# Kernel optimization log

Hardware: AMD Instinct MI355X
Metric: run time of the kernel (lower is better)

## Reference

```python
import jax, jax.numpy as jnp
import numpy as np

N_NODES = 100000
N_EDGES = 1600000
N_REL = 8
IN_CH = 64
HIDDEN = 64
OUT_CH = 32


def setup_inputs() -> dict:
    key = jax.random.key(0)
    ks = jax.random.split(key, 10)
    s_in = 1.0 / np.sqrt(IN_CH)
    s_h = 1.0 / np.sqrt(HIDDEN)
    return {
        "x": jax.random.normal(ks[0], (N_NODES, IN_CH), dtype=jnp.float32),
        "edge_index": jax.random.randint(ks[1], (2, N_EDGES), 0, N_NODES, dtype=jnp.int64),
        "edge_type": jax.random.randint(ks[2], (N_EDGES,), 0, N_REL, dtype=jnp.int64),
        "W0": jax.random.normal(ks[3], (N_REL, IN_CH, HIDDEN), dtype=jnp.float32) * s_in,
        "Q0": jax.random.normal(ks[4], (HIDDEN, 1), dtype=jnp.float32) * s_h,
        "K0": jax.random.normal(ks[5], (HIDDEN, 1), dtype=jnp.float32) * s_h,
        "b0": jnp.zeros((HIDDEN,), dtype=jnp.float32),
        "W1": jax.random.normal(ks[6], (N_REL, HIDDEN, OUT_CH), dtype=jnp.float32) * s_h,
        "Q1": jax.random.normal(ks[7], (OUT_CH, 1), dtype=jnp.float32) * (1.0 / np.sqrt(OUT_CH)),
        "K1": jax.random.normal(ks[8], (OUT_CH, 1), dtype=jnp.float32) * (1.0 / np.sqrt(OUT_CH)),
        "b1": jnp.zeros((OUT_CH,), dtype=jnp.float32),
    }


def rgat_conv(x, src, dst, et, W, Q, K, b, n_nodes):
    # relation-typed transform of all nodes: [R, N, out]
    xw = jnp.einsum("ni,rio->rno", x, W)
    # per-node, per-relation attention logits (heads=1, dim=1)
    q = jnp.einsum("rno,od->rnd", xw, Q)[..., 0]  # [R, N]
    k = jnp.einsum("rno,od->rnd", xw, K)[..., 0]  # [R, N]
    # additive self-attention, leaky_relu slope 0.2 (PyG RGATConv default)
    alpha = jax.nn.leaky_relu(q[et, dst] + k[et, src], negative_slope=0.2)  # [E]
    # across-relation segment softmax over incoming edges of each dst node
    amax = jax.ops.segment_max(alpha, dst, num_segments=n_nodes)
    a = jnp.exp(alpha - amax[dst])
    denom = jax.ops.segment_sum(a, dst, num_segments=n_nodes)
    a = a / (denom[dst] + 1e-16)
    # weighted scatter-add aggregation of transformed source features
    msg = a[:, None] * xw[et, src]  # [E, out]
    return jax.ops.segment_sum(msg, dst, num_segments=n_nodes) + b


def reference(x, edge_index, edge_type, W0, Q0, K0, b0, W1, Q1, K1, b1):
    src, dst = edge_index[0], edge_index[1]
    n = x.shape[0]
    h = rgat_conv(x, src, dst, edge_type, W0, Q0, K0, b0, n)
    h = jax.nn.relu(h)  # dropout p=0.0 -> identity
    out = rgat_conv(h, src, dst, edge_type, W1, Q1, K1, b1, n)
    return out
```

## Files before the change

kernel.cpp:

```cpp
#include <hip/hip_runtime.h>
#include <hip/hip_bf16.h>
#include <math.h>


#define CSR_CHUNK 8192

__global__ void k_bhist(const int* __restrict__ dst, int* __restrict__ bcount,
                        int E, int NB) {
    __shared__ int h[512];
    int t = threadIdx.x;
    for (int i = t; i < NB; i += 256) h[i] = 0;
    __syncthreads();
    int e0 = blockIdx.x * CSR_CHUNK;
    int e1 = min(e0 + CSR_CHUNK, E);
    for (int i = e0 + t; i < e1; i += 256) atomicAdd(&h[dst[i] >> 8], 1);
    __syncthreads();
    for (int i = t; i < NB; i += 256) {
        int c = h[i];
        if (c) atomicAdd(&bcount[i], c);
    }
}

__global__ void k_bscan(const int* __restrict__ bcount, int* __restrict__ bstart,
                        int* __restrict__ gcur, int* __restrict__ rowptr,
                        int NB, int N, int E) {
    __shared__ int s[512];
    int t = threadIdx.x;
    int v = (t < NB) ? bcount[t] : 0;
    s[t] = v;
    __syncthreads();
    for (int off = 1; off < 512; off <<= 1) {
        int a = (t >= off) ? s[t - off] : 0;
        __syncthreads();
        s[t] += a;
        __syncthreads();
    }
    int excl = s[t] - v;
    if (t < NB) {
        bstart[t] = excl;
        gcur[t] = excl;
    }
    if (t == 0) {
        bstart[NB] = E;
        rowptr[N] = E;
    }
}

__global__ void k_bscatter(const int* __restrict__ src, const int* __restrict__ dst,
                           const int* __restrict__ et, int* __restrict__ gcur,
                           unsigned* __restrict__ ebuf, int E, int NB) {
    __shared__ int h[512];
    __shared__ int basearr[512];
    int t = threadIdx.x;
    for (int i = t; i < NB; i += 256) h[i] = 0;
    __syncthreads();
    int e0 = blockIdx.x * CSR_CHUNK;
    int e1 = min(e0 + CSR_CHUNK, E);
    for (int i = e0 + t; i < e1; i += 256) atomicAdd(&h[dst[i] >> 8], 1);
    __syncthreads();
    for (int i = t; i < NB; i += 256) {
        int c = h[i];
        basearr[i] = c ? atomicAdd(&gcur[i], c) : 0;
        h[i] = 0;
    }
    __syncthreads();
    for (int i = e0 + t; i < e1; i += 256) {
        int d = dst[i];
        int b = d >> 8;
        int off = atomicAdd(&h[b], 1);
        ebuf[basearr[b] + off] =
            ((unsigned)(d & 255) << 20) | ((unsigned)et[i] << 17) | (unsigned)src[i];
    }
}

__global__ void k_bsort(const unsigned* __restrict__ ebuf, const int* __restrict__ bstart,
                        int* __restrict__ rowptr, int* __restrict__ csr, int N) {
    __shared__ int lh[256];
    __shared__ int ls[256];
    __shared__ int ss[256];
    int b = blockIdx.x, t = threadIdx.x;
    int e0 = bstart[b], e1 = bstart[b + 1];
    lh[t] = 0;
    __syncthreads();
    for (int i = e0 + t; i < e1; i += 256) atomicAdd(&lh[(ebuf[i] >> 20) & 255], 1);
    __syncthreads();
    int v = lh[t];
    ss[t] = v;
    __syncthreads();
    for (int off = 1; off < 256; off <<= 1) {
        int a = (t >= off) ? ss[t - off] : 0;
        __syncthreads();
        ss[t] += a;
        __syncthreads();
    }
    ls[t] = ss[t] - v;
    int node = b * 256 + t;
    if (node < N) rowptr[node] = e0 + ls[t];
    lh[t] = 0;
    __syncthreads();
    for (int i = e0 + t; i < e1; i += 256) {
        unsigned u = ebuf[i];
        int d = (u >> 20) & 255;
        int off = atomicAdd(&lh[d], 1);
        csr[e0 + ls[d] + off] = (int)(u & 0xFFFFF);
    }
}


__global__ void k_cast(const float4* __restrict__ in, ushort4* __restrict__ out, int n4) {
    int i = blockIdx.x * blockDim.x + threadIdx.x;
    if (i < n4) {
        float4 v = in[i];
        __hip_bfloat16 a = __float2bfloat16(v.x);
        __hip_bfloat16 b = __float2bfloat16(v.y);
        __hip_bfloat16 c = __float2bfloat16(v.z);
        __hip_bfloat16 d = __float2bfloat16(v.w);
        ushort4 o;
        o.x = *(unsigned short*)&a;
        o.y = *(unsigned short*)&b;
        o.z = *(unsigned short*)&c;
        o.w = *(unsigned short*)&d;
        out[i] = o;
    }
}


__global__ void k_wt2(const float* __restrict__ W, __hip_bfloat16* __restrict__ hi,
                      __hip_bfloat16* __restrict__ lo, int OUT, int total) {
    int t = blockIdx.x * blockDim.x + threadIdx.x;
    if (t < total) {
        int per = 64 * OUT;
        int r = t / per;
        int rem = t % per;
        int i = rem / OUT;
        int o = rem % OUT;
        float v = W[t];
        __hip_bfloat16 h = __float2bfloat16(v);
        __hip_bfloat16 l = __float2bfloat16(v - __bfloat162float(h));
        size_t idx = (size_t)o * 512 + i * 8 + r;
        hi[idx] = h;
        lo[idx] = l;
    }
}

__global__ void k_wqk(const float* W, const float* Qv, const float* Kv,
                      float* wq, float* wk, int OUT) {
    int t = blockIdx.x * blockDim.x + threadIdx.x;
    if (t < 8 * 64) {
        int r = t >> 6, i = t & 63;
        const float* wrow = W + ((size_t)r * 64 + i) * OUT;
        float a = 0.f, b = 0.f;
        for (int o = 0; o < OUT; o++) {
            float w = wrow[o];
            a += w * Qv[o];
            b += w * Kv[o];
        }
        wq[t] = a;
        wk[t] = b;
    }
}

__global__ void k_qk(const float* __restrict__ xin, const float* __restrict__ wq,
                     const float* __restrict__ wk, float* __restrict__ qn,
                     float* __restrict__ kn, int N) {
    __shared__ float sq[8 * 65], sk[8 * 65];
    int t = threadIdx.x;
    for (int idx = t; idx < 8 * 64; idx += blockDim.x) {
        int r = idx >> 6, i = idx & 63;
        sq[r * 65 + i] = wq[idx];
        sk[r * 65 + i] = wk[idx];
    }
    __syncthreads();
    int g = blockIdx.x * blockDim.x + t;
    if (g < N * 8) {
        int n = g >> 3, r = g & 7;
        const float* xp = xin + (size_t)n * 64;
        float qa = 0.f, ka = 0.f;
#pragma unroll
        for (int i = 0; i < 64; i++) {
            float xv = xp[i];
            qa += xv * sq[r * 65 + i];
            ka += xv * sk[r * 65 + i];
        }
        qn[g] = qa;
        kn[g] = ka;
    }
}

__global__ void k_agg2(const int* __restrict__ rowptr, const int* __restrict__ csr,
                       const float* __restrict__ qn, const float* __restrict__ kn,
                       const unsigned short* __restrict__ xb,
                       __hip_bfloat16* __restrict__ z, int N) {
    int wid = (blockIdx.x * blockDim.x + threadIdx.x) >> 6;
    int lane = threadIdx.x & 63;
    if (wid >= N) return;
    int r0 = rowptr[wid], r1 = rowptr[wid + 1];

    float qv = (lane < 8) ? qn[wid * 8 + lane] : 0.f;

    float denom = 0.f;
    float a0 = 0.f, a1 = 0.f, a2 = 0.f, a3 = 0.f;
    float a4 = 0.f, a5 = 0.f, a6 = 0.f, a7 = 0.f;

    for (int base = r0; base < r1; base += 64) {
        int s = base + lane;
        int pk = (s < r1) ? csr[s] : 0;
        int src = pk & 0x1FFFF;
        int rel = pk >> 17;
        float q = __shfl(qv, rel, 64);
        float tv = 0.f;
        if (s < r1) {
            float v = q + kn[src * 8 + rel];
            v = (v >= 0.f) ? v : 0.2f * v;
            tv = __expf(v);
        }
        float ts = tv;
#pragma unroll
        for (int off = 32; off > 0; off >>= 1) ts += __shfl_xor(ts, off, 64);
        denom += ts;

        int cnt = min(64, r1 - base);
        int tvi = (int)__float_as_uint(tv);
        for (int j = 0; j < cnt; j += 8) {
            unsigned p[8];
            float t[8];
#pragma unroll
            for (int u = 0; u < 8; u++) {
                p[u] = (unsigned)__builtin_amdgcn_readlane(pk, j + u);
                t[u] = __uint_as_float((unsigned)__builtin_amdgcn_readlane(tvi, j + u));
            }
            unsigned xu[8];
#pragma unroll
            for (int u = 0; u < 8; u++)
                xu[u] = (unsigned)xb[(size_t)(p[u] & 0x1FFFF) * 64 + lane];
#pragma unroll
            for (int u = 0; u < 8; u++) {
                float xv = __uint_as_float(xu[u] << 16);
                float tj = t[u];
                switch (p[u] >> 17) {
                    case 0: a0 += tj * xv; break;
                    case 1: a1 += tj * xv; break;
                    case 2: a2 += tj * xv; break;
                    case 3: a3 += tj * xv; break;
                    case 4: a4 += tj * xv; break;
                    case 5: a5 += tj * xv; break;
                    case 6: a6 += tj * xv; break;
                    case 7: a7 += tj * xv; break;
                }
            }
        }
    }

    float inv = 1.f / (denom + 1e-16f);
    unsigned short u[8];
    float av[8] = {a0, a1, a2, a3, a4, a5, a6, a7};
#pragma unroll
    for (int r = 0; r < 8; r++) {
        __hip_bfloat16 b = __float2bfloat16(av[r] * inv);
        u[r] = *(unsigned short*)&b;
    }
    uint4 pack;
    pack.x = (unsigned)u[0] | ((unsigned)u[1] << 16);
    pack.y = (unsigned)u[2] | ((unsigned)u[3] << 16);
    pack.z = (unsigned)u[4] | ((unsigned)u[5] << 16);
    pack.w = (unsigned)u[6] | ((unsigned)u[7] << 16);
    *(uint4*)((unsigned short*)z + (size_t)wid * 512 + lane * 8) = pack;
}

template <int OUT, bool RELU>
__global__ __launch_bounds__(256) void k_zw(
        const __hip_bfloat16* __restrict__ z,
        const __hip_bfloat16* __restrict__ wthi, const __hip_bfloat16* __restrict__ wtlo,
        const float* __restrict__ bias, float* __restrict__ xout,
        unsigned short* __restrict__ bout, int N) {
    using v8s = __attribute__((ext_vector_type(8))) short;
    using v4f = __attribute__((ext_vector_type(4))) float;
    constexpr int NT = OUT / 16;
    int wave = threadIdx.x >> 6;
    int lane = threadIdx.x & 63;
    int quad = lane >> 4;
    int l15 = lane & 15;
    int m0 = (blockIdx.x * 4 + wave) * 32;
    if (m0 >= N) return;

    v4f acc[NT][2];
#pragma unroll
    for (int nt = 0; nt < NT; nt++) {
        acc[nt][0] = (v4f){0.f, 0.f, 0.f, 0.f};
        acc[nt][1] = (v4f){0.f, 0.f, 0.f, 0.f};
    }

    const short* zp = (const short*)z;
    const short* wh = (const short*)wthi;
    const short* wl = (const short*)wtlo;
    int n0 = m0 + l15, n1 = m0 + 16 + l15;

    for (int k0 = 0; k0 < 512; k0 += 32) {
        int koff = k0 + quad * 8;
        v8s A0 = {}, A1 = {};
        if (n0 < N) A0 = *(const v8s*)(zp + (size_t)n0 * 512 + koff);
        if (n1 < N) A1 = *(const v8s*)(zp + (size_t)n1 * 512 + koff);
#pragma unroll
        for (int nt = 0; nt < NT; nt++) {
            v8s bh = *(const v8s*)(wh + (size_t)(nt * 16 + l15) * 512 + koff);
            v8s bl = *(const v8s*)(wl + (size_t)(nt * 16 + l15) * 512 + koff);
            acc[nt][0] = __builtin_amdgcn_mfma_f32_16x16x32_bf16(A0, bh, acc[nt][0], 0, 0, 0);
            acc[nt][0] = __builtin_amdgcn_mfma_f32_16x16x32_bf16(A0, bl, acc[nt][0], 0, 0, 0);
            acc[nt][1] = __builtin_amdgcn_mfma_f32_16x16x32_bf16(A1, bh, acc[nt][1], 0, 0, 0);
            acc[nt][1] = __builtin_amdgcn_mfma_f32_16x16x32_bf16(A1, bl, acc[nt][1], 0, 0, 0);
        }
    }

#pragma unroll
    for (int nt = 0; nt < NT; nt++) {
        float bcol = bias[nt * 16 + l15];
#pragma unroll
        for (int mm = 0; mm < 2; mm++) {
#pragma unroll
            for (int g = 0; g < 4; g++) {
                int row = m0 + mm * 16 + quad * 4 + g;
                if (row < N) {
                    float o = acc[nt][mm][g] + bcol;
                    if (RELU) o = fmaxf(o, 0.f);
                    xout[(size_t)row * OUT + nt * 16 + l15] = o;
                    if (bout) {
                        __hip_bfloat16 ob = __float2bfloat16(o);
                        bout[(size_t)row * OUT + nt * 16 + l15] = *(unsigned short*)&ob;
                    }
                }
            }
        }
    }
}


extern "C" void kernel_launch(void* const* d_in, const int* in_sizes, int n_in,
                              void* d_out, int out_size, void* d_ws, size_t ws_size,
                              hipStream_t stream) {
    const float* x   = (const float*)d_in[0];
    const int*   ei  = (const int*)d_in[1];
    const int*   et  = (const int*)d_in[2];
    const float* W0  = (const float*)d_in[3];
    const float* Q0  = (const float*)d_in[4];
    const float* K0  = (const float*)d_in[5];
    const float* b0  = (const float*)d_in[6];
    const float* W1  = (const float*)d_in[7];
    const float* Q1  = (const float*)d_in[8];
    const float* K1  = (const float*)d_in[9];
    const float* b1  = (const float*)d_in[10];
    float* out = (float*)d_out;

    const int N = in_sizes[0] / 64;
    const int E = in_sizes[2];
    const int* src = ei;
    const int* dst = ei + E;
    const int NB = (N + 255) >> 8;

    char* p = (char*)d_ws;
    auto alloc = [&](size_t bytes) -> void* {
        void* r = (void*)p;
        p += ((bytes + 255) / 256) * 256;
        return r;
    };
    int* rowptr   = (int*)alloc((size_t)(N + 1) * 4);
    int* bcount   = (int*)alloc((size_t)NB * 4);
    int* bstart   = (int*)alloc((size_t)(NB + 1) * 4);
    int* gcur     = (int*)alloc((size_t)NB * 4);
    unsigned* ebuf = (unsigned*)alloc((size_t)E * 4);
    int* csr      = (int*)alloc((size_t)E * 4);
    float* wq     = (float*)alloc(8 * 64 * 4);
    float* wk     = (float*)alloc(8 * 64 * 4);
    float* qn     = (float*)alloc((size_t)N * 8 * 4);
    float* kn     = (float*)alloc((size_t)N * 8 * 4);
    __hip_bfloat16* wthi = (__hip_bfloat16*)alloc((size_t)64 * 512 * 2);
    __hip_bfloat16* wtlo = (__hip_bfloat16*)alloc((size_t)64 * 512 * 2);
    __hip_bfloat16* z    = (__hip_bfloat16*)alloc((size_t)N * 512 * 2);
    float* h      = (float*)alloc((size_t)N * 64 * 4);
    unsigned short* xbb = (unsigned short*)alloc((size_t)N * 64 * 2);

    int nchunks = (E + CSR_CHUNK - 1) / CSR_CHUNK;
    hipMemsetAsync(bcount, 0, (size_t)NB * 4, stream);
    k_bhist<<<nchunks, 256, 0, stream>>>(dst, bcount, E, NB);
    k_bscan<<<1, 512, 0, stream>>>(bcount, bstart, gcur, rowptr, NB, N, E);
    k_bscatter<<<nchunks, 256, 0, stream>>>(src, dst, et, gcur, ebuf, E, NB);
    k_bsort<<<NB, 256, 0, stream>>>(ebuf, bstart, rowptr, csr, N);

    int naggb = (N * 64 + 255) / 256;
    int nzwb = (N + 127) / 128;
    int n4 = N * 64 / 4;

    k_wqk<<<2, 256, 0, stream>>>(W0, Q0, K0, wq, wk, 64);
    k_qk<<<(N * 8 + 255) / 256, 256, 0, stream>>>(x, wq, wk, qn, kn, N);
    k_cast<<<(n4 + 255) / 256, 256, 0, stream>>>((const float4*)x, (ushort4*)xbb, n4);
    k_wt2<<<(8 * 64 * 64 + 255) / 256, 256, 0, stream>>>(W0, wthi, wtlo, 64, 8 * 64 * 64);
    k_agg2<<<naggb, 256, 0, stream>>>(rowptr, csr, qn, kn, xbb, z, N);
    k_zw<64, true><<<nzwb, 256, 0, stream>>>(z, wthi, wtlo, b0, h, xbb, N);

    k_wqk<<<2, 256, 0, stream>>>(W1, Q1, K1, wq, wk, 32);
    k_qk<<<(N * 8 + 255) / 256, 256, 0, stream>>>(h, wq, wk, qn, kn, N);
    k_wt2<<<(8 * 64 * 32 + 255) / 256, 256, 0, stream>>>(W1, wthi, wtlo, 32, 8 * 64 * 32);
    k_agg2<<<naggb, 256, 0, stream>>>(rowptr, csr, qn, kn, xbb, z, N);
    k_zw<32, false><<<nzwb, 256, 0, stream>>>(z, wthi, wtlo, b1, out, nullptr, N);
}
```

Before: 501.0 us.

## Fuse bf16 cast into tiled qk kernel, shrink CSR buckets, unroll aggregation wider

Replaces the standalone cast kernel and per-thread qk kernel with a tiled kernel that stages node features in LDS, computes q/k logits and writes the bf16 copy in one pass; the bf16 write is removed from the dense transform epilogue. CSR bucketing uses 128-node buckets and smaller edge chunks for more blocks. The aggregation loop gathers 16 neighbors per iteration instead of 8 to expose more memory parallelism, at the cost of more registers.

Result: slower. 524.1 us (+4.6%).

```diff
diff --git a/kernel.cpp b/kernel.cpp
--- a/kernel.cpp
+++ b/kernel.cpp
@@ -3,17 +3,17 @@
 #include <math.h>
 
 
-#define CSR_CHUNK 8192
+#define CSR_CHUNK 2048
 
 __global__ void k_bhist(const int* __restrict__ dst, int* __restrict__ bcount,
                         int E, int NB) {
-    __shared__ int h[512];
+    __shared__ int h[1024];
     int t = threadIdx.x;
     for (int i = t; i < NB; i += 256) h[i] = 0;
     __syncthreads();
     int e0 = blockIdx.x * CSR_CHUNK;
     int e1 = min(e0 + CSR_CHUNK, E);
-    for (int i = e0 + t; i < e1; i += 256) atomicAdd(&h[dst[i] >> 8], 1);
+    for (int i = e0 + t; i < e1; i += 256) atomicAdd(&h[dst[i] >> 7], 1);
     __syncthreads();
     for (int i = t; i < NB; i += 256) {
         int c = h[i];
@@ -24,12 +24,12 @@
 __global__ void k_bscan(const int* __restrict__ bcount, int* __restrict__ bstart,
                         int* __restrict__ gcur, int* __restrict__ rowptr,
                         int NB, int N, int E) {
-    __shared__ int s[512];
+    __shared__ int s[1024];
     int t = threadIdx.x;
     int v = (t < NB) ? bcount[t] : 0;
     s[t] = v;
     __syncthreads();
-    for (int off = 1; off < 512; off <<= 1) {
+    for (int off = 1; off < 1024; off <<= 1) {
         int a = (t >= off) ? s[t - off] : 0;
         __syncthreads();
         s[t] += a;
@@ -49,14 +49,14 @@
 __global__ void k_bscatter(const int* __restrict__ src, const int* __restrict__ dst,
                            const int* __restrict__ et, int* __restrict__ gcur,
                            unsigned* __restrict__ ebuf, int E, int NB) {
-    __shared__ int h[512];
-    __shared__ int basearr[512];
+    __shared__ int h[1024];
+    __shared__ int basearr[1024];
     int t = threadIdx.x;
     for (int i = t; i < NB; i += 256) h[i] = 0;
     __syncthreads();
     int e0 = blockIdx.x * CSR_CHUNK;
     int e1 = min(e0 + CSR_CHUNK, E);
-    for (int i = e0 + t; i < e1; i += 256) atomicAdd(&h[dst[i] >> 8], 1);
+    for (int i = e0 + t; i < e1; i += 256) atomicAdd(&h[dst[i] >> 7], 1);
     __syncthreads();
     for (int i = t; i < NB; i += 256) {
         int c = h[i];
@@ -66,10 +66,10 @@
     __syncthreads();
     for (int i = e0 + t; i < e1; i += 256) {
         int d = dst[i];
-        int b = d >> 8;
+        int b = d >> 7;
         int off = atomicAdd(&h[b], 1);
         ebuf[basearr[b] + off] =
-            ((unsigned)(d & 255) << 20) | ((unsigned)et[i] << 17) | (unsigned)src[i];
+            ((unsigned)(d & 127) << 20) | ((unsigned)et[i] << 17) | (unsigned)src[i];
     }
 }
 
@@ -82,7 +82,7 @@
     int e0 = bstart[b], e1 = bstart[b + 1];
     lh[t] = 0;
     __syncthreads();
-    for (int i = e0 + t; i < e1; i += 256) atomicAdd(&lh[(ebuf[i] >> 20) & 255], 1);
+    for (int i = e0 + t; i < e1; i += 256) atomicAdd(&lh[(ebuf[i] >> 20) & 127], 1);
     __syncthreads();
     int v = lh[t];
     ss[t] = v;
@@ -94,33 +94,15 @@
         __syncthreads();
     }
     ls[t] = ss[t] - v;
-    int node = b * 256 + t;
-    if (node < N) rowptr[node] = e0 + ls[t];
+    int node = b * 128 + t;
+    if (t < 128 && node < N) rowptr[node] = e0 + ls[t];
     lh[t] = 0;
     __syncthreads();
     for (int i = e0 + t; i < e1; i += 256) {
         unsigned u = ebuf[i];
-        int d = (u >> 20) & 255;
+        int d = (u >> 20) & 127;
         int off = atomicAdd(&lh[d], 1);
         csr[e0 + ls[d] + off] = (int)(u & 0xFFFFF);
-    }
-}
-
-
-__global__ void k_cast(const float4* __restrict__ in, ushort4* __restrict__ out, int n4) {
-    int i = blockIdx.x * blockDim.x + threadIdx.x;
-    if (i < n4) {
-        float4 v = in[i];
-        __hip_bfloat16 a = __float2bfloat16(v.x);
-        __hip_bfloat16 b = __float2bfloat16(v.y);
-        __hip_bfloat16 c = __float2bfloat16(v.z);
-        __hip_bfloat16 d = __float2bfloat16(v.w);
-        ushort4 o;
-        o.x = *(unsigned short*)&a;
-        o.y = *(unsigned short*)&b;
-        o.z = *(unsigned short*)&c;
-        o.w = *(unsigned short*)&d;
-        out[i] = o;
     }
 }
 
@@ -160,30 +142,58 @@
     }
 }
 
-__global__ void k_qk(const float* __restrict__ xin, const float* __restrict__ wq,
-                     const float* __restrict__ wk, float* __restrict__ qn,
-                     float* __restrict__ kn, int N) {
-    __shared__ float sq[8 * 65], sk[8 * 65];
+__global__ __launch_bounds__(256) void k_qk2(
+        const float* __restrict__ xin, const float* __restrict__ wq,
+        const float* __restrict__ wk, float* __restrict__ qn,
+        float* __restrict__ kn, unsigned short* __restrict__ xbb, int N) {
+    __shared__ float xt[64][65];
+    __shared__ float swq[8 * 65], swk[8 * 65];
     int t = threadIdx.x;
-    for (int idx = t; idx < 8 * 64; idx += blockDim.x) {
-        int r = idx >> 6, i = idx & 63;
-        sq[r * 65 + i] = wq[idx];
-        sk[r * 65 + i] = wk[idx];
-    }
-    __syncthreads();
-    int g = blockIdx.x * blockDim.x + t;
-    if (g < N * 8) {
-        int n = g >> 3, r = g & 7;
-        const float* xp = xin + (size_t)n * 64;
-        float qa = 0.f, ka = 0.f;
-#pragma unroll
-        for (int i = 0; i < 64; i++) {
-            float xv = xp[i];
-            qa += xv * sq[r * 65 + i];
-            ka += xv * sk[r * 65 + i];
-        }
-        qn[g] = qa;
-        kn[g] = ka;
+    int nb0 = blockIdx.x * 64;
+    for (int i = t; i < 512; i += 256) {
+        int r = i >> 6, c = i & 63;
+        swq[r * 65 + c] = wq[i];
+        swk[r * 65 + c] = wk[i];
+    }
+    for (int i = t; i < 1024; i += 256) {
+        int ns = i >> 4;
+        int c4 = i & 15;
+        int n = nb0 + ns;
+        float4 v = {0.f, 0.f, 0.f, 0.f};
+        if (n < N) v = ((const float4*)xin)[(size_t)n * 16 + c4];
+        xt[ns][c4 * 4 + 0] = v.x;
+        xt[ns][c4 * 4 + 1] = v.y;
+        xt[ns][c4 * 4 + 2] = v.z;
+        xt[ns][c4 * 4 + 3] = v.w;
+        if (n < N) {
+            __hip_bfloat16 b0 = __float2bfloat16(v.x);
+            __hip_bfloat16 b1 = __float2bfloat16(v.y);
+            __hip_bfloat16 b2 = __float2bfloat16(v.z);
+            __hip_bfloat16 b3 = __float2bfloat16(v.w);
+            ushort4 o;
+            o.x = *(unsigned short*)&b0;
+            o.y = *(unsigned short*)&b1;
+            o.z = *(unsigned short*)&b2;
+            o.w = *(unsigned short*)&b3;
+            *(ushort4*)(xbb + (size_t)n * 64 + c4 * 4) = o;
+        }
+    }
+    __syncthreads();
+#pragma unroll
+    for (int g = t; g < 512; g += 256) {
+        int ns = g >> 3, r = g & 7;
+        int n = nb0 + ns;
+        if (n < N) {
+            float qa = 0.f, ka = 0.f;
+#pragma unroll
+            for (int i = 0; i < 64; i++) {
+                float xv = xt[ns][i];
+                qa += xv * swq[r * 65 + i];
+                ka += xv * swk[r * 65 + i];
+            }
+            qn[(size_t)n * 8 + r] = qa;
+            kn[(size_t)n * 8 + r] = ka;
+        }
     }
 }
 
@@ -221,20 +231,20 @@
 
         int cnt = min(64, r1 - base);
         int tvi = (int)__float_as_uint(tv);
-        for (int j = 0; j < cnt; j += 8) {
-            unsigned p[8];
-            float t[8];
-#pragma unroll
-            for (int u = 0; u < 8; u++) {
+        for (int j = 0; j < cnt; j += 16) {
+            unsigned p[16];
+            float t[16];
+#pragma unroll
+            for (int u = 0; u < 16; u++) {
                 p[u] = (unsigned)__builtin_amdgcn_readlane(pk, j + u);
                 t[u] = __uint_as_float((unsigned)__builtin_amdgcn_readlane(tvi, j + u));
             }
-            unsigned xu[8];
-#pragma unroll
-            for (int u = 0; u < 8; u++)
+            unsigned xu[16];
+#pragma unroll
+            for (int u = 0; u < 16; u++)
                 xu[u] = (unsigned)xb[(size_t)(p[u] & 0x1FFFF) * 64 + lane];
 #pragma unroll
-            for (int u = 0; u < 8; u++) {
+            for (int u = 0; u < 16; u++) {
                 float xv = __uint_as_float(xu[u] << 16);
                 float tj = t[u];
                 switch (p[u] >> 17) {
@@ -271,8 +281,7 @@
 __global__ __launch_bounds__(256) void k_zw(
         const __hip_bfloat16* __restrict__ z,
         const __hip_bfloat16* __restrict__ wthi, const __hip_bfloat16* __restrict__ wtlo,
-        const float* __restrict__ bias, float* __restrict__ xout,
-        unsigned short* __restrict__ bout, int N) {
+        const float* __restrict__ bias, float* __restrict__ xout, int N) {
     using v8s = __attribute__((ext_vector_type(8))) short;
     using v4f = __attribute__((ext_vector_type(4))) float;
     constexpr int NT = OUT / 16;
@@ -323,10 +332,6 @@
                     float o = acc[nt][mm][g] + bcol;
                     if (RELU) o = fmaxf(o, 0.f);
                     xout[(size_t)row * OUT + nt * 16 + l15] = o;
-                    if (bout) {
-                        __hip_bfloat16 ob = __float2bfloat16(o);
-                        bout[(size_t)row * OUT + nt * 16 + l15] = *(unsigned short*)&ob;
-                    }
                 }
             }
         }
@@ -354,7 +359,7 @@
     const int E = in_sizes[2];
     const int* src = ei;
     const int* dst = ei + E;
-    const int NB = (N + 255) >> 8;
+    const int NB = (N + 127) >> 7;
 
     char* p = (char*)d_ws;
     auto alloc = [&](size_t bytes) -> void* {
@@ -363,9 +368,9 @@
         return r;
     };
     int* rowptr   = (int*)alloc((size_t)(N + 1) * 4);
-    int* bcount   = (int*)alloc((size_t)NB * 4);
-    int* bstart   = (int*)alloc((size_t)(NB + 1) * 4);
-    int* gcur     = (int*)alloc((size_t)NB * 4);
+    int* bcount   = (int*)alloc(1025 * 4);
+    int* bstart   = (int*)alloc(1025 * 4);
+    int* gcur     = (int*)alloc(1025 * 4);
     unsigned* ebuf = (unsigned*)alloc((size_t)E * 4);
     int* csr      = (int*)alloc((size_t)E * 4);
     float* wq     = (float*)alloc(8 * 64 * 4);
@@ -381,24 +386,23 @@
     int nchunks = (E + CSR_CHUNK - 1) / CSR_CHUNK;
     hipMemsetAsync(bcount, 0, (size_t)NB * 4, stream);
     k_bhist<<<nchunks, 256, 0, stream>>>(dst, bcount, E, NB);
-    k_bscan<<<1, 512, 0, stream>>>(bcount, bstart, gcur, rowptr, NB, N, E);
+    k_bscan<<<1, 1024, 0, stream>>>(bcount, bstart, gcur, rowptr, NB, N, E);
     k_bscatter<<<nchunks, 256, 0, stream>>>(src, dst, et, gcur, ebuf, E, NB);
     k_bsort<<<NB, 256, 0, stream>>>(ebuf, bstart, rowptr, csr, N);
 
     int naggb = (N * 64 + 255) / 256;
     int nzwb = (N + 127) / 128;
-    int n4 = N * 64 / 4;
+    int nqkb = (N + 63) / 64;
 
     k_wqk<<<2, 256, 0, stream>>>(W0, Q0, K0, wq, wk, 64);
-    k_qk<<<(N * 8 + 255) / 256, 256, 0, stream>>>(x, wq, wk, qn, kn, N);
-    k_cast<<<(n4 + 255) / 256, 256, 0, stream>>>((const float4*)x, (ushort4*)xbb, n4);
+    k_qk2<<<nqkb, 256, 0, stream>>>(x, wq, wk, qn, kn, xbb, N);
     k_wt2<<<(8 * 64 * 64 + 255) / 256, 256, 0, stream>>>(W0, wthi, wtlo, 64, 8 * 64 * 64);
     k_agg2<<<naggb, 256, 0, stream>>>(rowptr, csr, qn, kn, xbb, z, N);
-    k_zw<64, true><<<nzwb, 256, 0, stream>>>(z, wthi, wtlo, b0, h, xbb, N);
+    k_zw<64, true><<<nzwb, 256, 0, stream>>>(z, wthi, wtlo, b0, h, N);
 
     k_wqk<<<2, 256, 0, stream>>>(W1, Q1, K1, wq, wk, 32);
-    k_qk<<<(N * 8 + 255) / 256, 256, 0, stream>>>(h, wq, wk, qn, kn, N);
+    k_qk2<<<nqkb, 256, 0, stream>>>(h, wq, wk, qn, kn, xbb, N);
     k_wt2<<<(8 * 64 * 32 + 255) / 256, 256, 0, stream>>>(W1, wthi, wtlo, 32, 8 * 64 * 32);
     k_agg2<<<naggb, 256, 0, stream>>>(rowptr, csr, qn, kn, xbb, z, N);
-    k_zw<32, false><<<nzwb, 256, 0, stream>>>(z, wthi, wtlo, b1, out, nullptr, N);
-}
+    k_zw<32, false><<<nzwb, 256, 0, stream>>>(z, wthi, wtlo, b1, out, N);
+}
```
